# Optimization experiments

Hardware: AMD Instinct MI355X
Metric: run time of the kernel (lower is better)

The kernel has to match this reference:

```python
import jax, jax.numpy as jnp
import numpy as np

B, T, D, H, OUT = 64, 2048, 40, 164, 7


def _lstm_layer(xs, lengths, W_ih, W_hh, b):
    """xs: [T,B,Din] -> (all hiddens [T,B,H], last valid hidden [B,H]).

    Matches packed-sequence semantics: state stops updating once t >= length,
    so the final carry h equals the hidden at each sequence's last real step.
    PyTorch gate order: i, f, g, o.
    """
    Tt, Bb, _ = xs.shape
    gx = jnp.einsum('tbd,gd->tbg', xs, W_ih) + b  # input projections, one big GEMM

    def step(carry, inp):
        h, c = carry
        g_t, t = inp
        gates = g_t + h @ W_hh.T
        i, f, g, o = jnp.split(gates, 4, axis=-1)
        c_new = jax.nn.sigmoid(f) * c + jax.nn.sigmoid(i) * jnp.tanh(g)
        h_new = jax.nn.sigmoid(o) * jnp.tanh(c_new)
        m = (t < lengths)[:, None]  # freeze state past each sequence's length
        return (jnp.where(m, h_new, h), jnp.where(m, c_new, c)), jnp.where(m, h_new, h)

    z = jnp.zeros((Bb, W_hh.shape[1]), xs.dtype)
    (hT, _), hs = jax.lax.scan(step, (z, z), (gx, jnp.arange(Tt)))
    return hs, hT


def setup_inputs() -> dict:
    key = jax.random.key(0)
    ks = jax.random.split(key, 16)
    s = 1.0 / np.sqrt(H)
    inp = {
        'x': jax.random.normal(ks[0], (B, T, D), jnp.float32),
        'lengths': jax.random.randint(ks[1], (B,), 1, T + 1, jnp.int32),
        'W_ih_0': jax.random.normal(ks[2], (4 * H, D), jnp.float32) * s,
        'W_hh_0': jax.random.normal(ks[3], (4 * H, H), jnp.float32) * s,
        'b_0': jax.random.normal(ks[4], (4 * H,), jnp.float32) * s,
        'W_ih_1': jax.random.normal(ks[5], (4 * H, H), jnp.float32) * s,
        'W_hh_1': jax.random.normal(ks[6], (4 * H, H), jnp.float32) * s,
        'b_1': jax.random.normal(ks[7], (4 * H,), jnp.float32) * s,
        'W_ih_2': jax.random.normal(ks[8], (4 * H, H), jnp.float32) * s,
        'W_hh_2': jax.random.normal(ks[9], (4 * H, H), jnp.float32) * s,
        'b_2': jax.random.normal(ks[10], (4 * H,), jnp.float32) * s,
        'fc_w': jax.random.normal(ks[11], (OUT, H), jnp.float32) * s,
        'fc_b': jax.random.normal(ks[12], (OUT,), jnp.float32) * s,
    }
    return inp


def reference(x, lengths, W_ih_0, W_hh_0, b_0, W_ih_1, W_hh_1, b_1,
              W_ih_2, W_hh_2, b_2, fc_w, fc_b):
    xs = jnp.swapaxes(x, 0, 1)  # [T,B,D] for time-major scan
    hs, _ = _lstm_layer(xs, lengths, W_ih_0, W_hh_0, b_0)
    hs, _ = _lstm_layer(hs, lengths, W_ih_1, W_hh_1, b_1)
    _, hT = _lstm_layer(hs, lengths, W_ih_2, W_hh_2, b_2)  # hidden[-1]
    return hT @ fc_w.T + fc_b  # [B, OUT]
```

## Files before the change

kernel.cpp:

```cpp
#include <hip/hip_runtime.h>
#include <stdint.h>


#define TT 2048
#define BB 64
#define GG 656
#define HH 164
#define EP 176
#define GP 704
#define KPH 192
#define KPD 96
#define CC 128
#define NCH (TT/CC)
#define TSL 8
#define NSL (CC/TSL)

typedef _Float16 half2v __attribute__((ext_vector_type(2)));
typedef _Float16 half8  __attribute__((ext_vector_type(8)));
typedef float    f32x4  __attribute__((ext_vector_type(4)));

#define SZ_WIH   ((size_t)3*GG*KPH*2)
#define SZ_WHH   ((size_t)3*GP*KPH*2)
#define SZ_GX1   ((size_t)3*16*CC*GG*4*2)
#define GX_SLOT_HALVES ((size_t)3*16*CC*GG*4)
#define SZ_HR    ((size_t)2*2*BB*CC*96*4)
#define HR_DW    (2*2*BB*CC*96)
#define SZ_SC    ((size_t)3*BB*HH*4)
#define SZ_SH    ((size_t)3*BB*96*4)

#define LOG2E 1.4426950408889634f

__device__ __forceinline__ float fexp2(float x) {
#if __has_builtin(__builtin_amdgcn_exp2f)
  return __builtin_amdgcn_exp2f(x);
#else
  float r; asm("v_exp_f32 %0, %1" : "=v"(r) : "v"(x)); return r;
#endif
}
__device__ __forceinline__ float frcp(float x) {
#if __has_builtin(__builtin_amdgcn_rcpf)
  return __builtin_amdgcn_rcpf(x);
#else
  float r; asm("v_rcp_f32 %0, %1" : "=v"(r) : "v"(x)); return r;
#endif
}
__device__ __forceinline__ float sigmf(float x) {
  return frcp(1.0f + fexp2(-LOG2E * x));
}
__device__ __forceinline__ float tanhf_(float x) {
  return __builtin_fmaf(-2.0f, frcp(1.0f + fexp2(2.0f * LOG2E * x)), 1.0f);
}

__global__ void kprep_w(const float* wih0, const float* whh0,
                        const float* wih1, const float* whh1,
                        const float* wih2, const float* whh2,
                        _Float16* wih16, _Float16* whh16) {
  int i = threadIdx.x + blockIdx.x * blockDim.x;
  if (i >= 3*GP*KPH) return;
  int l = i / (GP*KPH);
  int r2 = i - l*(GP*KPH);
  int prow = r2 / KPH;
  int k = r2 - prow*KPH;
  const float* wihl = (l == 0) ? wih0 : ((l == 1) ? wih1 : wih2);
  const float* whhl = (l == 0) ? whh0 : ((l == 1) ? whh1 : whh2);
  int g = prow / EP, e = prow - g*EP;
  float vh = 0.f;
  if (e < HH && k < HH) vh = whhl[(size_t)(g*HH + e)*HH + k];
  whh16[((size_t)l*GP + prow)*KPH + k] = (_Float16)vh;
  if (prow < GG) {
    float vi = 0.f;
    if (l == 0) { if (k < 40) vi = wihl[(size_t)prow*40 + k]; }
    else        { if (k < HH) vi = wihl[(size_t)prow*HH + k]; }
    wih16[((size_t)l*GG + prow)*KPH + k] = (_Float16)vi;
  }
}

__global__ void kzero(uint32_t* p, int n) {
  int i = threadIdx.x + blockIdx.x * blockDim.x;
  if (i < n) p[i] = 0u;
}

__device__ __forceinline__ void gemm_body(
    int l, int bg, int ts, int ch, const int* lengths, const float* x,
    const uint32_t* wihw, const uint32_t* hring, const float* bp,
    uint16_t* gxs, uint32_t* smem, int tid) {
  int maxlen = 1;
  #pragma unroll
  for (int bi = 0; bi < 16; ++bi) {
    int L = lengths[bg*16 + bi]; if (L < 1) L = 1; if (L > TT) L = TT;
    if (L > maxlen) maxlen = L;
  }
  const int tb = ts*TSL;
  const int t0 = ch*CC + tb;
  if (t0 >= maxlen) return;
  int tcnt = maxlen - t0; if (tcnt > TSL) tcnt = TSL;

  if (l == 0) {
    for (int idx = tid; idx < TSL*16*96; idx += 704) {
      int tloc = idx / 1536, r = idx - tloc*1536, b = r / 96, dw = r - b*96;
      uint32_t v = 0;
      if (dw < 20) {
        const float* xs = x + ((size_t)(bg*16 + b)*TT + (t0 + tloc))*40 + dw*2;
        half2v pp; pp[0] = (_Float16)xs[0]; pp[1] = (_Float16)xs[1];
        v = __builtin_bit_cast(uint32_t, pp);
      }
      smem[(tloc*16 + b)*100 + dw] = v;
    }
  } else {
    const uint32_t* hbs = hring + ((size_t)((l-1)*2 + (ch & 1))*BB)*CC*96;
    for (int idx = tid; idx < TSL*16*96; idx += 704) {
      int tloc = idx / 1536, r = idx - tloc*1536, b = r / 96, dw = r - b*96;
      smem[(tloc*16 + b)*100 + dw] =
          hbs[((size_t)(bg*16 + b)*CC + tb + tloc)*96 + dw];
    }
  }
  __syncthreads();

  const int lane = tid & 63, wv = tid >> 6;
  const int quad = lane >> 4, n15 = lane & 15;
  uint16_t* gxo = gxs + (((size_t)(l*16 + bg*4 + quad)*CC + tb)*GG)*4;

  half8 wf[4][6];
  float bv[4] = {0.f, 0.f, 0.f, 0.f};
  #pragma unroll
  for (int ni = 0; ni < 4; ++ni) {
    int nt = wv + ni*11;
    if (nt < 41) {
      int wrow = nt*16 + n15;
      const half8* bsrc = (const half8*)(wihw + ((size_t)l*GG + wrow)*KPD);
      #pragma unroll
      for (int kk = 0; kk < 6; ++kk) wf[ni][kk] = bsrc[kk*4 + quad];
      bv[ni] = bp[wrow];
    }
  }

  for (int tloc = 0; tloc < tcnt; ++tloc) {
    const half8* asrc = (const half8*)(smem + tloc*1600);
    half8 af[6];
    #pragma unroll
    for (int kk = 0; kk < 6; ++kk) af[kk] = asrc[n15*25 + kk*4 + quad];
    #pragma unroll
    for (int ni = 0; ni < 4; ++ni) {
      int nt = wv + ni*11;
      if (nt < 41) {
        int wrow = nt*16 + n15;
        f32x4 a0 = {0.f,0.f,0.f,0.f};
        #pragma unroll
        for (int kk = 0; kk < 6; ++kk)
          a0 = __builtin_amdgcn_mfma_f32_16x16x32_f16(af[kk], wf[ni][kk], a0, 0, 0, 0);
        half2v p0; p0[0] = (_Float16)(a0[0] + bv[ni]); p0[1] = (_Float16)(a0[1] + bv[ni]);
        half2v p1; p1[0] = (_Float16)(a0[2] + bv[ni]); p1[1] = (_Float16)(a0[3] + bv[ni]);
        uint2 pk;
        pk.x = __builtin_bit_cast(uint32_t, p0);
        pk.y = __builtin_bit_cast(uint32_t, p1);
        *(uint2*)(gxo + ((size_t)tloc*GG + wrow)*4) = pk;
      }
    }
  }
}

__device__ __forceinline__ void rec_body(
    int l, int bg, int ch, const int* lengths,
    const uint32_t* whhw, const uint16_t* gxs, uint32_t* hring,
    float* state_c, uint32_t* state_h, uint32_t* smem, int tid) {

  const int gb0 = bg*4;
  int maxlen = 1;
  #pragma unroll
  for (int bi = 0; bi < 4; ++bi) {
    int L = lengths[gb0 + bi]; if (L < 1) L = 1; if (L > TT) L = TT;
    if (L > maxlen) maxlen = L;
  }
  const int t0 = ch*CC;
  if (t0 >= maxlen) return;
  int t1 = t0 + CC; if (t1 > maxlen) t1 = maxlen;
  const int nst = t1 - t0;

  const int wv = tid >> 6, ln = tid & 63;
  const int quad = ln >> 4, n15 = ln & 15;
  const int e = wv*16 + n15;
  const int evalid = (e < HH);
  const int gb = gb0 + quad;

  int lenq = lengths[gb]; if (lenq < 1) lenq = 1; if (lenq > TT) lenq = TT;

  half8 wB[24];
  {
    const half8* wb8 = (const half8*)(whhw + (size_t)l*GP*KPD);
    #pragma unroll
    for (int g = 0; g < 4; ++g) {
      int row = g*EP + e;
      #pragma unroll
      for (int kk = 0; kk < 6; ++kk)
        wB[g*6 + kk] = wb8[(size_t)row*24 + kk*4 + quad];
    }
  }

  float creg = 0.f;
  if (ch > 0 && evalid)
    creg = state_c[((size_t)l*BB + gb)*HH + e];

  uint32_t* hb0 = smem;
  uint32_t* hb1 = smem + 1600;
  for (int i2 = tid; i2 < 1600; i2 += 704) {
    int bb = i2 / 100, dd = i2 - bb*100;
    uint32_t v = 0;
    if (dd < 96 && ch > 0) v = state_h[((size_t)l*BB + gb0 + (bb >> 2))*96 + dd];
    hb0[i2] = v; hb1[i2] = v;
  }
  __syncthreads();

  uint16_t hbit = ((const uint16_t*)hb0)[(quad*4)*200 + e];

  const uint16_t* gpt = gxs + (((size_t)(l*16 + bg)*CC)*GG)*4
                            + (size_t)e*4 + quad;
  uint16_t gxv[4];
  #pragma unroll
  for (int g = 0; g < 4; ++g) gxv[g] = gpt[g*(HH*4)];
  gpt += GG*4;

  const int dorb = (l < 2);
  uint16_t* rp;
  {
    uint16_t* hrb16 = (uint16_t*)(hring + ((size_t)(l*2 + (ch & 1))*BB)*CC*96);
    rp = hrb16 + ((size_t)gb*CC)*192 + e;
  }

  const int lo = n15*100 + quad*4;
  const int ho_off = (quad*4)*200 + e;

  int p = 0;
  for (int it = 0; it < nst; ++it) {
    const int t = t0 + it;
    uint32_t* hin  = p ? hb1 : hb0;
    uint32_t* hout = p ? hb0 : hb1;

    float gxf0 = (float)__builtin_bit_cast(_Float16, gxv[0]);
    float gxf1 = (float)__builtin_bit_cast(_Float16, gxv[1]);
    float gxf2 = (float)__builtin_bit_cast(_Float16, gxv[2]);
    float gxf3 = (float)__builtin_bit_cast(_Float16, gxv[3]);
    #pragma unroll
    for (int g = 0; g < 4; ++g) gxv[g] = gpt[g*(HH*4)];
    gpt += GG*4;

    f32x4 acc0, acc1, acc2, acc3;
    {
      const f32x4 z = {0.f, 0.f, 0.f, 0.f};
      half8 af = *(const half8*)&hin[lo];
      acc0 = __builtin_amdgcn_mfma_f32_16x16x32_f16(af, wB[0],  z, 0, 0, 0);
      acc1 = __builtin_amdgcn_mfma_f32_16x16x32_f16(af, wB[6],  z, 0, 0, 0);
      acc2 = __builtin_amdgcn_mfma_f32_16x16x32_f16(af, wB[12], z, 0, 0, 0);
      acc3 = __builtin_amdgcn_mfma_f32_16x16x32_f16(af, wB[18], z, 0, 0, 0);
    }
    #pragma unroll
    for (int kk = 1; kk < 6; ++kk) {
      half8 af = *(const half8*)&hin[lo + kk*16];
      acc0 = __builtin_amdgcn_mfma_f32_16x16x32_f16(af, wB[kk],      acc0, 0, 0, 0);
      acc1 = __builtin_amdgcn_mfma_f32_16x16x32_f16(af, wB[6 + kk],  acc1, 0, 0, 0);
      acc2 = __builtin_amdgcn_mfma_f32_16x16x32_f16(af, wB[12 + kk], acc2, 0, 0, 0);
      acc3 = __builtin_amdgcn_mfma_f32_16x16x32_f16(af, wB[18 + kk], acc3, 0, 0, 0);
    }
    {
      float gi = acc0[0] + gxf0;
      float gf = acc1[0] + gxf1;
      float gg2 = acc2[0] + gxf2;
      float go = acc3[0] + gxf3;
      float cn = sigmf(gf)*creg + sigmf(gi)*tanhf_(gg2);
      float hv = sigmf(go)*tanhf_(cn);
      if (t < lenq) {
        creg = cn;
        _Float16 h16 = (_Float16)hv;
        hbit = __builtin_bit_cast(uint16_t, h16);
      }
      if (evalid) {
        ((uint16_t*)hout)[ho_off] = hbit;
        if (dorb) *rp = hbit;
      }
      rp += 192;
    }
    asm volatile("s_waitcnt lgkmcnt(0)" ::: "memory");
    __builtin_amdgcn_s_barrier();
    p ^= 1;
  }

  uint32_t* hfin = p ? hb1 : hb0;
  uint32_t* shb = state_h + ((size_t)l*BB + gb0)*96;
  for (int i2 = tid; i2 < 4*96; i2 += 704) {
    int bb = i2 / 96, dd = i2 - bb*96;
    shb[(size_t)bb*96 + dd] = hfin[(bb*4)*100 + dd];
  }
  if (evalid)
    state_c[((size_t)l*BB + gb)*HH + e] = creg;
}

__global__ __launch_bounds__(704, 1) void kstep_f(
    int j, const int* lengths, const float* x,
    const uint32_t* wihw, const uint32_t* whhw,
    const float* b0, const float* b1, const float* b2,
    uint16_t* gx, uint32_t* hring, float* state_c, uint32_t* state_h) {
  __shared__ __align__(16) uint32_t smem[TSL*1600];
  const int blk = blockIdx.x, tid = threadIdx.x;
  if (blk < 192) {
    const int l = blk >> 6, r = blk & 63, bg = r >> 4, ts = r & 15;
    const int ch = j - 2*l;
    if (ch < 0 || ch >= NCH) return;
    const float* bp = (l == 0) ? b0 : ((l == 1) ? b1 : b2);
    uint16_t* gxs = gx + (size_t)(ch & 1)*GX_SLOT_HALVES;
    gemm_body(l, bg, ts, ch, lengths, x, wihw, hring, bp, gxs, smem, tid);
  } else {
    const int idx = blk - 192;
    if (idx >= 48) return;
    const int l = idx >> 4, bg = idx & 15;
    const int ch = j - 2*l - 1;
    if (ch < 0 || ch >= NCH) return;
    const uint16_t* gxs = gx + (size_t)(ch & 1)*GX_SLOT_HALVES;
    rec_body(l, bg, ch, lengths, whhw, gxs, hring,
             state_c, state_h, smem, tid);
  }
}

__global__ __launch_bounds__(704, 1) void kgemm_s(
    int step, const int* lengths, const float* x,
    const uint32_t* wihw, const float* b0, const float* b1, const float* b2,
    uint16_t* gx, const uint32_t* hring) {
  __shared__ __align__(16) uint32_t smem[TSL*1600];
  const int blk = blockIdx.x;
  const int l = blk >> 6, r = blk & 63, bg = r >> 4, ts = r & 15;
  const int ch = step - l;
  if (ch < 0 || ch >= NCH) return;
  const float* bp = (l == 0) ? b0 : ((l == 1) ? b1 : b2);
  gemm_body(l, bg, ts, ch, lengths, x, wihw, hring, bp, gx, smem, threadIdx.x);
}

__global__ __launch_bounds__(704, 1) void krec_s(
    int step, const int* lengths,
    const uint32_t* whhw, const uint16_t* gx, uint32_t* hring,
    float* state_c, uint32_t* state_h) {
  __shared__ __align__(16) uint32_t smem[TSL*1600];
  const int idx = blockIdx.x;
  const int l = idx >> 4, bg = idx & 15;
  const int ch = step - l;
  if (ch < 0 || ch >= NCH) return;
  rec_body(l, bg, ch, lengths, whhw, gx, hring,
           state_c, state_h, smem, threadIdx.x);
}

__global__ void kfc(const float* fcw, const float* fcb,
                    const uint32_t* state_h, float* out) {
  int b = blockIdx.x, o = threadIdx.x;
  if (o >= 7) return;
  const uint16_t* h16 = (const uint16_t*)(state_h + (size_t)(2*BB + b)*96);
  float s = fcb[o];
  for (int m = 0; m < HH; ++m) {
    _Float16 hv = __builtin_bit_cast(_Float16, h16[m]);
    s += fcw[o*HH + m] * (float)hv;
  }
  out[b*7 + o] = s;
}

extern "C" void kernel_launch(void* const* d_in, const int* in_sizes, int n_in,
                              void* d_out, int out_size, void* d_ws, size_t ws_size,
                              hipStream_t stream) {
  const float* x      = (const float*)d_in[0];
  const int*  lengths = (const int*)  d_in[1];
  const float* wih0   = (const float*)d_in[2];
  const float* whh0   = (const float*)d_in[3];
  const float* b0     = (const float*)d_in[4];
  const float* wih1   = (const float*)d_in[5];
  const float* whh1   = (const float*)d_in[6];
  const float* b1     = (const float*)d_in[7];
  const float* wih2   = (const float*)d_in[8];
  const float* whh2   = (const float*)d_in[9];
  const float* b2     = (const float*)d_in[10];
  const float* fcw    = (const float*)d_in[11];
  const float* fcb    = (const float*)d_in[12];

  const size_t off_wih = 0;
  const size_t off_whh = SZ_WIH;
  const size_t off_gx  = SZ_WIH + SZ_WHH;
  const size_t tail    = SZ_HR + SZ_SC + SZ_SH;
  const size_t need_fused = off_gx + 2*SZ_GX1 + tail;
  const size_t need_seq   = off_gx + 1*SZ_GX1 + tail;
  const int fused = (ws_size >= need_fused);
  if (!fused && ws_size < need_seq) return;
  const size_t gx_bytes = fused ? 2*SZ_GX1 : SZ_GX1;
  const size_t off_hr = off_gx + gx_bytes;
  const size_t off_sc = off_hr + SZ_HR;
  const size_t off_sh = off_sc + SZ_SC;

  char* ws = (char*)d_ws;
  _Float16* wih16 = (_Float16*)(ws + off_wih);
  _Float16* whh16 = (_Float16*)(ws + off_whh);
  uint16_t* gxw   = (uint16_t*)(ws + off_gx);
  uint32_t* hrw   = (uint32_t*)(ws + off_hr);
  float*    scw   = (float*)   (ws + off_sc);
  uint32_t* shw   = (uint32_t*)(ws + off_sh);

  hipLaunchKernelGGL(kprep_w, dim3((3*GP*KPH + 255)/256), dim3(256), 0, stream,
                     wih0, whh0, wih1, whh1, wih2, whh2, wih16, whh16);
  hipLaunchKernelGGL(kzero, dim3((HR_DW + 255)/256), dim3(256), 0, stream,
                     hrw, HR_DW);

  if (fused) {
    for (int jj = 0; jj <= NCH + 4; ++jj) {
      hipLaunchKernelGGL(kstep_f, dim3(240), dim3(704), 0, stream,
                         jj, lengths, x, (const uint32_t*)wih16,
                         (const uint32_t*)whh16, b0, b1, b2,
                         gxw, hrw, scw, shw);
    }
  } else {
    for (int i = 0; i < NCH + 2; ++i) {
      hipLaunchKernelGGL(kgemm_s, dim3(192), dim3(704), 0, stream,
                         i, lengths, x, (const uint32_t*)wih16,
                         b0, b1, b2, gxw, (const uint32_t*)hrw);
      hipLaunchKernelGGL(krec_s, dim3(48), dim3(704), 0, stream,
                         i, lengths, (const uint32_t*)whh16,
                         (const uint16_t*)gxw, hrw, scw, shw);
    }
  }

  hipLaunchKernelGGL(kfc, dim3(64), dim3(64), 0, stream,
                     fcw, fcb, shw, (float*)d_out);
}
```

Measured before the change: 2.314 ms.

## Process two batch groups per recurrent block to interleave independent chains

Each recurrent block now handles two 4-sequence batch groups (pp and pp+8) with the same register-resident W_hh. The two independent MFMA chains and gate computations sit between a single barrier per timestep, halving the recurrent block count. The aim is to hide MFMA and LDS latency on the serial critical path and cut barrier overhead per unit of work. The cost is a longer per-step body, and each block now runs until the longer of the two groups' max length.

```diff
diff --git a/kernel.cpp b/kernel.cpp
--- a/kernel.cpp
+++ b/kernel.cpp
@@ -159,17 +159,20 @@
   }
 }
 
-__device__ __forceinline__ void rec_body(
-    int l, int bg, int ch, const int* lengths,
+__device__ __forceinline__ void rec_pair_body(
+    int l, int pp, int ch, const int* lengths,
     const uint32_t* whhw, const uint16_t* gxs, uint32_t* hring,
     float* state_c, uint32_t* state_h, uint32_t* smem, int tid) {
 
-  const int gb0 = bg*4;
+  const int bgA = pp, bgB = pp + 8;
+  const int gb0A = bgA*4, gb0B = bgB*4;
   int maxlen = 1;
   #pragma unroll
   for (int bi = 0; bi < 4; ++bi) {
-    int L = lengths[gb0 + bi]; if (L < 1) L = 1; if (L > TT) L = TT;
-    if (L > maxlen) maxlen = L;
+    int LA = lengths[gb0A + bi]; if (LA < 1) LA = 1; if (LA > TT) LA = TT;
+    int LB = lengths[gb0B + bi]; if (LB < 1) LB = 1; if (LB > TT) LB = TT;
+    if (LA > maxlen) maxlen = LA;
+    if (LB > maxlen) maxlen = LB;
   }
   const int t0 = ch*CC;
   if (t0 >= maxlen) return;
@@ -180,9 +183,10 @@
   const int quad = ln >> 4, n15 = ln & 15;
   const int e = wv*16 + n15;
   const int evalid = (e < HH);
-  const int gb = gb0 + quad;
-
-  int lenq = lengths[gb]; if (lenq < 1) lenq = 1; if (lenq > TT) lenq = TT;
+  const int gbA = gb0A + quad, gbB = gb0B + quad;
+
+  int lenqA = lengths[gbA]; if (lenqA < 1) lenqA = 1; if (lenqA > TT) lenqA = TT;
+  int lenqB = lengths[gbB]; if (lenqB < 1) lenqB = 1; if (lenqB > TT) lenqB = TT;
 
   half8 wB[24];
   {
@@ -196,34 +200,46 @@
     }
   }
 
-  float creg = 0.f;
-  if (ch > 0 && evalid)
-    creg = state_c[((size_t)l*BB + gb)*HH + e];
-
-  uint32_t* hb0 = smem;
-  uint32_t* hb1 = smem + 1600;
+  float cregA = 0.f, cregB = 0.f;
+  if (ch > 0 && evalid) {
+    cregA = state_c[((size_t)l*BB + gbA)*HH + e];
+    cregB = state_c[((size_t)l*BB + gbB)*HH + e];
+  }
+
+  uint32_t* hA0 = smem;
+  uint32_t* hA1 = smem + 1600;
+  uint32_t* hB0 = smem + 3200;
+  uint32_t* hB1 = smem + 4800;
   for (int i2 = tid; i2 < 1600; i2 += 704) {
     int bb = i2 / 100, dd = i2 - bb*100;
-    uint32_t v = 0;
-    if (dd < 96 && ch > 0) v = state_h[((size_t)l*BB + gb0 + (bb >> 2))*96 + dd];
-    hb0[i2] = v; hb1[i2] = v;
+    uint32_t vA = 0, vB = 0;
+    if (dd < 96 && ch > 0) {
+      vA = state_h[((size_t)l*BB + gb0A + (bb >> 2))*96 + dd];
+      vB = state_h[((size_t)l*BB + gb0B + (bb >> 2))*96 + dd];
+    }
+    hA0[i2] = vA; hA1[i2] = vA;
+    hB0[i2] = vB; hB1[i2] = vB;
   }
   __syncthreads();
 
-  uint16_t hbit = ((const uint16_t*)hb0)[(quad*4)*200 + e];
-
-  const uint16_t* gpt = gxs + (((size_t)(l*16 + bg)*CC)*GG)*4
-                            + (size_t)e*4 + quad;
-  uint16_t gxv[4];
+  uint16_t hbitA = ((const uint16_t*)hA0)[(quad*4)*200 + e];
+  uint16_t hbitB = ((const uint16_t*)hB0)[(quad*4)*200 + e];
+
+  const uint16_t* gptA = gxs + (((size_t)(l*16 + bgA)*CC)*GG)*4
+                             + (size_t)e*4 + quad;
+  const uint16_t* gptB = gxs + (((size_t)(l*16 + bgB)*CC)*GG)*4
+                             + (size_t)e*4 + quad;
+  uint16_t gxvA[4], gxvB[4];
   #pragma unroll
-  for (int g = 0; g < 4; ++g) gxv[g] = gpt[g*(HH*4)];
-  gpt += GG*4;
+  for (int g = 0; g < 4; ++g) { gxvA[g] = gptA[g*(HH*4)]; gxvB[g] = gptB[g*(HH*4)]; }
+  gptA += GG*4; gptB += GG*4;
 
   const int dorb = (l < 2);
-  uint16_t* rp;
+  uint16_t* rpA; uint16_t* rpB;
   {
     uint16_t* hrb16 = (uint16_t*)(hring + ((size_t)(l*2 + (ch & 1))*BB)*CC*96);
-    rp = hrb16 + ((size_t)gb*CC)*192 + e;
+    rpA = hrb16 + ((size_t)gbA*CC)*192 + e;
+    rpB = hrb16 + ((size_t)gbB*CC)*192 + e;
   }
 
   const int lo = n15*100 + quad*4;
@@ -232,65 +248,113 @@
   int p = 0;
   for (int it = 0; it < nst; ++it) {
     const int t = t0 + it;
-    uint32_t* hin  = p ? hb1 : hb0;
-    uint32_t* hout = p ? hb0 : hb1;
-
-    float gxf0 = (float)__builtin_bit_cast(_Float16, gxv[0]);
-    float gxf1 = (float)__builtin_bit_cast(_Float16, gxv[1]);
-    float gxf2 = (float)__builtin_bit_cast(_Float16, gxv[2]);
-    float gxf3 = (float)__builtin_bit_cast(_Float16, gxv[3]);
+    uint32_t* hinA  = p ? hA1 : hA0;
+    uint32_t* houtA = p ? hA0 : hA1;
+    uint32_t* hinB  = p ? hB1 : hB0;
+    uint32_t* houtB = p ? hB0 : hB1;
+
+    float gxfA0 = (float)__builtin_bit_cast(_Float16, gxvA[0]);
+    float gxfA1 = (float)__builtin_bit_cast(_Float16, gxvA[1]);
+    float gxfA2 = (float)__builtin_bit_cast(_Float16, gxvA[2]);
+    float gxfA3 = (float)__builtin_bit_cast(_Float16, gxvA[3]);
+    float gxfB0 = (float)__builtin_bit_cast(_Float16, gxvB[0]);
+    float gxfB1 = (float)__builtin_bit_cast(_Float16, gxvB[1]);
+    float gxfB2 = (float)__builtin_bit_cast(_Float16, gxvB[2]);
+    float gxfB3 = (float)__builtin_bit_cast(_Float16, gxvB[3]);
     #pragma unroll
-    for (int g = 0; g < 4; ++g) gxv[g] = gpt[g*(HH*4)];
-    gpt += GG*4;
-
-    f32x4 acc0, acc1, acc2, acc3;
+    for (int g = 0; g < 4; ++g) { gxvA[g] = gptA[g*(HH*4)]; gxvB[g] = gptB[g*(HH*4)]; }
+    gptA += GG*4; gptB += GG*4;
+
     {
-      const f32x4 z = {0.f, 0.f, 0.f, 0.f};
-      half8 af = *(const half8*)&hin[lo];
-      acc0 = __builtin_amdgcn_mfma_f32_16x16x32_f16(af, wB[0],  z, 0, 0, 0);
-      acc1 = __builtin_amdgcn_mfma_f32_16x16x32_f16(af, wB[6],  z, 0, 0, 0);
-      acc2 = __builtin_amdgcn_mfma_f32_16x16x32_f16(af, wB[12], z, 0, 0, 0);
-      acc3 = __builtin_amdgcn_mfma_f32_16x16x32_f16(af, wB[18], z, 0, 0, 0);
-    }
-    #pragma unroll
-    for (int kk = 1; kk < 6; ++kk) {
-      half8 af = *(const half8*)&hin[lo + kk*16];
-      acc0 = __builtin_amdgcn_mfma_f32_16x16x32_f16(af, wB[kk],      acc0, 0, 0, 0);
-      acc1 = __builtin_amdgcn_mfma_f32_16x16x32_f16(af, wB[6 + kk],  acc1, 0, 0, 0);
-      acc2 = __builtin_amdgcn_mfma_f32_16x16x32_f16(af, wB[12 + kk], acc2, 0, 0, 0);
-      acc3 = __builtin_amdgcn_mfma_f32_16x16x32_f16(af, wB[18 + kk], acc3, 0, 0, 0);
-    }
+      f32x4 acc0, acc1, acc2, acc3;
+      {
+        const f32x4 z = {0.f, 0.f, 0.f, 0.f};
+        half8 af = *(const half8*)&hinA[lo];
+        acc0 = __builtin_amdgcn_mfma_f32_16x16x32_f16(af, wB[0],  z, 0, 0, 0);
+        acc1 = __builtin_amdgcn_mfma_f32_16x16x32_f16(af, wB[6],  z, 0, 0, 0);
+        acc2 = __builtin_amdgcn_mfma_f32_16x16x32_f16(af, wB[12], z, 0, 0, 0);
+        acc3 = __builtin_amdgcn_mfma_f32_16x16x32_f16(af, wB[18], z, 0, 0, 0);
+      }
+      #pragma unroll
+      for (int kk = 1; kk < 6; ++kk) {
+        half8 af = *(const half8*)&hinA[lo + kk*16];
+        acc0 = __builtin_amdgcn_mfma_f32_16x16x32_f16(af, wB[kk],      acc0, 0, 0, 0);
+        acc1 = __builtin_amdgcn_mfma_f32_16x16x32_f16(af, wB[6 + kk],  acc1, 0, 0, 0);
+        acc2 = __builtin_amdgcn_mfma_f32_16x16x32_f16(af, wB[12 + kk], acc2, 0, 0, 0);
+        acc3 = __builtin_amdgcn_mfma_f32_16x16x32_f16(af, wB[18 + kk], acc3, 0, 0, 0);
+      }
+      float gi = acc0[0] + gxfA0;
+      float gf = acc1[0] + gxfA1;
+      float gg2 = acc2[0] + gxfA2;
+      float go = acc3[0] + gxfA3;
+      float cn = sigmf(gf)*cregA + sigmf(gi)*tanhf_(gg2);
+      float hv = sigmf(go)*tanhf_(cn);
+      if (t < lenqA) {
+        cregA = cn;
+        _Float16 h16 = (_Float16)hv;
+        hbitA = __builtin_bit_cast(uint16_t, h16);
+      }
+      if (evalid) {
+        ((uint16_t*)houtA)[ho_off] = hbitA;
+        if (dorb) *rpA = hbitA;
+      }
+      rpA += 192;
+    }
+
     {
-      float gi = acc0[0] + gxf0;
-      float gf = acc1[0] + gxf1;
-      float gg2 = acc2[0] + gxf2;
-      float go = acc3[0] + gxf3;
-      float cn = sigmf(gf)*creg + sigmf(gi)*tanhf_(gg2);
+      f32x4 acc0, acc1, acc2, acc3;
+      {
+        const f32x4 z = {0.f, 0.f, 0.f, 0.f};
+        half8 af = *(const half8*)&hinB[lo];
+        acc0 = __builtin_amdgcn_mfma_f32_16x16x32_f16(af, wB[0],  z, 0, 0, 0);
+        acc1 = __builtin_amdgcn_mfma_f32_16x16x32_f16(af, wB[6],  z, 0, 0, 0);
+        acc2 = __builtin_amdgcn_mfma_f32_16x16x32_f16(af, wB[12], z, 0, 0, 0);
+        acc3 = __builtin_amdgcn_mfma_f32_16x16x32_f16(af, wB[18], z, 0, 0, 0);
+      }
+      #pragma unroll
+      for (int kk = 1; kk < 6; ++kk) {
+        half8 af = *(const half8*)&hinB[lo + kk*16];
+        acc0 = __builtin_amdgcn_mfma_f32_16x16x32_f16(af, wB[kk],      acc0, 0, 0, 0);
+        acc1 = __builtin_amdgcn_mfma_f32_16x16x32_f16(af, wB[6 + kk],  acc1, 0, 0, 0);
+        acc2 = __builtin_amdgcn_mfma_f32_16x16x32_f16(af, wB[12 + kk], acc2, 0, 0, 0);
+        acc3 = __builtin_amdgcn_mfma_f32_16x16x32_f16(af, wB[18 + kk], acc3, 0, 0, 0);
+      }
+      float gi = acc0[0] + gxfB0;
+      float gf = acc1[0] + gxfB1;
+      float gg2 = acc2[0] + gxfB2;
+      float go = acc3[0] + gxfB3;
+      float cn = sigmf(gf)*cregB + sigmf(gi)*tanhf_(gg2);
       float hv = sigmf(go)*tanhf_(cn);
-      if (t < lenq) {
-        creg = cn;
+      if (t < lenqB) {
+        cregB = cn;
         _Float16 h16 = (_Float16)hv;
-        hbit = __builtin_bit_cast(uint16_t, h16);
+        hbitB = __builtin_bit_cast(uint16_t, h16);
       }
       if (evalid) {
-        ((uint16_t*)hout)[ho_off] = hbit;
-        if (dorb) *rp = hbit;
-      }
-      rp += 192;
-    }
+        ((uint16_t*)houtB)[ho_off] = hbitB;
+        if (dorb) *rpB = hbitB;
+      }
+      rpB += 192;
+    }
+
     asm volatile("s_waitcnt lgkmcnt(0)" ::: "memory");
     __builtin_amdgcn_s_barrier();
     p ^= 1;
   }
 
-  uint32_t* hfin = p ? hb1 : hb0;
-  uint32_t* shb = state_h + ((size_t)l*BB + gb0)*96;
+  uint32_t* hfinA = p ? hA1 : hA0;
+  uint32_t* hfinB = p ? hB1 : hB0;
+  uint32_t* shbA = state_h + ((size_t)l*BB + gb0A)*96;
+  uint32_t* shbB = state_h + ((size_t)l*BB + gb0B)*96;
   for (int i2 = tid; i2 < 4*96; i2 += 704) {
     int bb = i2 / 96, dd = i2 - bb*96;
-    shb[(size_t)bb*96 + dd] = hfin[(bb*4)*100 + dd];
-  }
-  if (evalid)
-    state_c[((size_t)l*BB + gb)*HH + e] = creg;
+    shbA[(size_t)bb*96 + dd] = hfinA[(bb*4)*100 + dd];
+    shbB[(size_t)bb*96 + dd] = hfinB[(bb*4)*100 + dd];
+  }
+  if (evalid) {
+    state_c[((size_t)l*BB + gbA)*HH + e] = cregA;
+    state_c[((size_t)l*BB + gbB)*HH + e] = cregB;
+  }
 }
 
 __global__ __launch_bounds__(704, 1) void kstep_f(
@@ -309,13 +373,13 @@
     gemm_body(l, bg, ts, ch, lengths, x, wihw, hring, bp, gxs, smem, tid);
   } else {
     const int idx = blk - 192;
-    if (idx >= 48) return;
-    const int l = idx >> 4, bg = idx & 15;
+    if (idx >= 24) return;
+    const int l = idx >> 3, pp = idx & 7;
     const int ch = j - 2*l - 1;
     if (ch < 0 || ch >= NCH) return;
     const uint16_t* gxs = gx + (size_t)(ch & 1)*GX_SLOT_HALVES;
-    rec_body(l, bg, ch, lengths, whhw, gxs, hring,
-             state_c, state_h, smem, tid);
+    rec_pair_body(l, pp, ch, lengths, whhw, gxs, hring,
+                  state_c, state_h, smem, tid);
   }
 }
 
@@ -338,11 +402,11 @@
     float* state_c, uint32_t* state_h) {
   __shared__ __align__(16) uint32_t smem[TSL*1600];
   const int idx = blockIdx.x;
-  const int l = idx >> 4, bg = idx & 15;
+  const int l = idx >> 3, pp = idx & 7;
   const int ch = step - l;
   if (ch < 0 || ch >= NCH) return;
-  rec_body(l, bg, ch, lengths, whhw, gx, hring,
-           state_c, state_h, smem, threadIdx.x);
+  rec_pair_body(l, pp, ch, lengths, whhw, gx, hring,
+                state_c, state_h, smem, threadIdx.x);
 }
 
 __global__ void kfc(const float* fcw, const float* fcb,
@@ -403,7 +467,7 @@
 
   if (fused) {
     for (int jj = 0; jj <= NCH + 4; ++jj) {
-      hipLaunchKernelGGL(kstep_f, dim3(240), dim3(704), 0, stream,
+      hipLaunchKernelGGL(kstep_f, dim3(216), dim3(704), 0, stream,
                          jj, lengths, x, (const uint32_t*)wih16,
                          (const uint32_t*)whh16, b0, b1, b2,
                          gxw, hrw, scw, shw);
@@ -413,7 +477,7 @@
       hipLaunchKernelGGL(kgemm_s, dim3(192), dim3(704), 0, stream,
                          i, lengths, x, (const uint32_t*)wih16,
                          b0, b1, b2, gxw, (const uint32_t*)hrw);
-      hipLaunchKernelGGL(krec_s, dim3(48), dim3(704), 0, stream,
+      hipLaunchKernelGGL(krec_s, dim3(24), dim3(704), 0, stream,
                          i, lengths, (const uint32_t*)whh16,
                          (const uint16_t*)gxw, hrw, scw, shw);
     }
```

New measurement: 4.591 ms. +98.4%, slower.
